# Performance work log

Hardware: AMD Instinct MI355X
Metric: run time of the kernel (lower is better)

## Reference

```python
import jax, jax.numpy as jnp
import numpy as np

N_GRAPHS = 512  # number of graphs in the batch
S2S_STEPS = 3   # Set2Set processing_steps


def segment_softmax(e, seg, num_seg):
    m = jax.ops.segment_max(e, seg, num_segments=num_seg)
    ex = jnp.exp(e - m[seg])
    s = jax.ops.segment_sum(ex, seg, num_segments=num_seg)
    return ex / s[seg]


def setup_inputs() -> dict:
    key = jax.random.key(0)
    ks = jax.random.split(key, 24)
    N, E, Fin, Fe, D = 30000, 480000, 25, 14, 256
    s = 0.05
    inp = {
        "x": jax.random.normal(ks[0], (N, Fin), jnp.float32),
        "edge_attr": jax.random.normal(ks[1], (E, Fe), jnp.float32),
        # lin0
        "W0": jax.random.normal(ks[2], (Fin, D), jnp.float32) * s,
        "b0": jnp.zeros((D,), jnp.float32),
        # DMPNN edge-message MLP: [x_src || e_attr] -> D -> D
        "Wm1": jax.random.normal(ks[3], (D + Fe, D), jnp.float32) * s,
        "bm1": jnp.zeros((D,), jnp.float32),
        "Wm2": jax.random.normal(ks[4], (D, D), jnp.float32) * s,
        "bm2": jnp.zeros((D,), jnp.float32),
        # node (root) update
        "Wr": jax.random.normal(ks[5], (D, D), jnp.float32) * s,
        "br": jnp.zeros((D,), jnp.float32),
        # Set2Set LSTM: input 2D -> hidden D
        "Wih": jax.random.normal(ks[6], (2 * D, 4 * D), jnp.float32) * s,
        "Whh": jax.random.normal(ks[7], (D, 4 * D), jnp.float32) * s,
        "bl": jnp.zeros((4 * D,), jnp.float32),
        # readout MLP
        "W1": jax.random.normal(ks[8], (2 * D, D), jnp.float32) * s,
        "b1": jnp.zeros((D,), jnp.float32),
        "W2": jax.random.normal(ks[9], (D, 1), jnp.float32) * s,
        "b2": jnp.zeros((1,), jnp.float32),
        "edge_index": jax.random.randint(ks[10], (2, E), 0, N, jnp.int32),
        "batch": jnp.sort(jax.random.randint(ks[11], (N,), 0, N_GRAPHS, jnp.int32)),
    }
    return inp


def reference(x, edge_attr, W0, b0, Wm1, bm1, Wm2, bm2, Wr, br,
              Wih, Whh, bl, W1, b1, W2, b2, edge_index, batch):
    N = x.shape[0]
    # lin0 + relu
    h0 = jax.nn.relu(x @ W0 + b0)  # [N, D]
    # DMPNNLayer2: edge-conditioned message, sum-aggregate, root update (eval: no dropout)
    src, dst = edge_index[0], edge_index[1]
    m = jax.nn.relu(jnp.concatenate([h0[src], edge_attr], axis=-1) @ Wm1 + bm1)  # [E, D]
    m = m @ Wm2 + bm2
    agg = jax.ops.segment_sum(m, dst, num_segments=N)  # [N, D]
    out = jax.nn.relu(h0 @ Wr + br + agg)  # relu in top-level forward, massage_depth=1
    # Set2Set pooling (processing_steps=3)
    D = out.shape[1]
    B = N_GRAPHS
    q_star = jnp.zeros((B, 2 * D), out.dtype)
    h = jnp.zeros((B, D), out.dtype)
    c = jnp.zeros((B, D), out.dtype)
    for _ in range(S2S_STEPS):
        gates = q_star @ Wih + h @ Whh + bl  # [B, 4D]
        i, f, g, o = jnp.split(gates, 4, axis=-1)
        c = jax.nn.sigmoid(f) * c + jax.nn.sigmoid(i) * jnp.tanh(g)
        h = jax.nn.sigmoid(o) * jnp.tanh(c)
        e = jnp.sum(out * h[batch], axis=-1)              # [N]
        a = segment_softmax(e, batch, B)                  # [N]
        r = jax.ops.segment_sum(a[:, None] * out, batch, num_segments=B)  # [B, D]
        q_star = jnp.concatenate([h, r], axis=-1)
    # readout (eval: dropout identity)
    y = jax.nn.relu(q_star @ W1 + b1)
    y = y @ W2 + b2
    return y.reshape(-1)
```

## Files before the change

### kernel.cpp

```cpp
#include <hip/hip_runtime.h>

typedef unsigned short u16;
typedef unsigned char u8;
typedef unsigned int u32;
using s16x8 = __attribute__((ext_vector_type(8))) short;
using f32x4 = __attribute__((ext_vector_type(4))) float;

#define DEV static __device__ __forceinline__

DEV float b2f(u16 u) { return __uint_as_float(((u32)u) << 16); }
DEV u16 f2bu(float f) {
    u32 u = __float_as_uint(f);
    u32 r = (u + 0x7FFFu + ((u >> 16) & 1u)) >> 16;
    return (u16)r;
}
DEV float sigm(float x) { return 1.0f / (1.0f + expf(-x)); }

DEV float ldv(const void* p, int i, int f32flag) {
    if (f32flag) return ((const float*)p)[i];
    return b2f(((const u16*)p)[i]);
}
DEV void stv(void* p, int i, float v, int f32flag) {
    if (f32flag) ((float*)p)[i] = v;
    else ((u16*)p)[i] = f2bu(v);
}

DEV int lower_bound(const int* b, int n, int v) {
    int lo = 0, hi = n;
    while (lo < hi) { int mid = (lo + hi) >> 1; if (b[mid] < v) lo = mid + 1; else hi = mid; }
    return lo;
}

__global__ void DMPNN_Change_678604832935_kernel(int* p) {
    if (p && threadIdx.x == 0 && blockIdx.x == 0) p[0] = 1;
}

__global__ void detect_kernel(const void* x, int* flag) {
    __shared__ int cnt[128];
    int tid = threadIdx.x;
    if (tid < 128) {
        u16 v = ((const u16*)x)[tid];
        int e = (v >> 7) & 0xFF;
        cnt[tid] = (e >= 100 && e <= 141) ? 1 : 0;
    }
    __syncthreads();
    if (tid == 0) {
        int s = 0;
        for (int i = 0; i < 128; ++i) s += cnt[i];
        flag[0] = (s < 110) ? 1 : 0;
    }
}

__global__ void fillv_kernel(void* out, const int* flag, float v) {
    int i = blockIdx.x * 256 + threadIdx.x;
    if (i < 512) stv(out, i, v, flag[0]);
}

__global__ void zero_kernel(float* p, int n) {
    int i = blockIdx.x * 256 + threadIdx.x;
    int stride = gridDim.x * 256;
    for (; i < n; i += stride) p[i] = 0.0f;
}

__global__ void hist_kernel(const int* __restrict__ eidx, u32* __restrict__ cnt) {
    int i = blockIdx.x * 256 + threadIdx.x;
    if (i < 480000) atomicAdd(&cnt[eidx[480000 + i]], 1u);
}

__global__ void scan1_kernel(const u32* __restrict__ cnt, u32* __restrict__ part) {
    __shared__ u32 s[256];
    int i = blockIdx.x * 256 + threadIdx.x;
    s[threadIdx.x] = (i < 30000) ? cnt[i] : 0u;
    __syncthreads();
    for (int st = 128; st > 0; st >>= 1) {
        if (threadIdx.x < st) s[threadIdx.x] += s[threadIdx.x + st];
        __syncthreads();
    }
    if (threadIdx.x == 0) part[blockIdx.x] = s[0];
}

__global__ void scan2_kernel(const u32* __restrict__ part, u32* __restrict__ pexcl, int nb) {
    if (threadIdx.x == 0 && blockIdx.x == 0) {
        u32 run = 0;
        for (int i = 0; i < nb; ++i) { pexcl[i] = run; run += part[i]; }
    }
}

__global__ void scan3_kernel(u32* __restrict__ cursor, const u32* __restrict__ pexcl) {
    __shared__ u32 s[256];
    int b = blockIdx.x, tid = threadIdx.x;
    int i = b * 256 + tid;
    u32 v = (i < 30000) ? cursor[i] : 0u;
    s[tid] = v;
    __syncthreads();
    for (int off = 1; off < 256; off <<= 1) {
        u32 t = (tid >= off) ? s[tid - off] : 0u;
        __syncthreads();
        s[tid] += t;
        __syncthreads();
    }
    u32 excl = s[tid] - v + pexcl[b];
    if (i < 30000) cursor[i] = excl;
}

__global__ void scatter_kernel(const int* __restrict__ eidx, u32* __restrict__ cursor,
                               u16* __restrict__ permLo, u8* __restrict__ permHi) {
    int i = blockIdx.x * 256 + threadIdx.x;
    if (i < 480000) {
        int d = eidx[480000 + i];
        u32 pos = atomicAdd(&cursor[d], 1u);
        permLo[pos] = (u16)(i & 0xFFFF);
        permHi[pos] = (u8)(i >> 16);
    }
}

__global__ void deg_kernel(const u32* __restrict__ cursor, float* __restrict__ degf) {
    int i = blockIdx.x * 256 + threadIdx.x;
    if (i < 30000) {
        u32 end = cursor[i];
        u32 beg = (i > 0) ? cursor[i - 1] : 0u;
        degf[i] = (float)(end - beg);
    }
}

__global__ void to_blocked(const void* src, int K, int ktiles, const int* flag,
                           u16* dst) {
    int idx = blockIdx.x * 256 + threadIdx.x;
    int total = ktiles * 4 * 256 * 8;
    if (idx >= total) return;
    int f32 = flag[0];
    int c = idx & 7;
    int n = (idx >> 3) & 255;
    int jk = idx >> 11;
    int j = jk & 3, kt = jk >> 2;
    int k = kt * 32 + j * 8 + c;
    u16 v = 0;
    if (k < K) v = f2bu(ldv(src, k * 256 + n, f32));
    dst[idx] = v;
}

__global__ void to_blocked2(const void* src1, int K1, const void* src2, int K2,
                            const int* flag, u16* dst) {
    int idx = blockIdx.x * 256 + threadIdx.x;
    int total = 24 * 4 * 1024 * 8;
    if (idx >= total) return;
    int f32 = flag[0];
    int c = idx & 7;
    int n = (idx >> 3) & 1023;
    int jk = idx >> 13;
    int j = jk & 3, kt = jk >> 2;
    int k = kt * 32 + j * 8 + c;
    u16 v = 0;
    if (k < K1) v = f2bu(ldv(src1, k * 1024 + n, f32));
    else if (k - K1 < K2) v = f2bu(ldv(src2, (k - K1) * 1024 + n, f32));
    dst[idx] = v;
}

__global__ __launch_bounds__(256) void lin0_kernel(const void* x, const void* W0,
                                                   const void* b0, const int* flag,
                                                   u16* h0b) {
    int f32 = flag[0];
    int n0 = blockIdx.x * 8, tid = threadIdx.x;
    __shared__ float xs[8][26];
    if (tid < 200) {
        int nn = tid / 25, k = tid % 25;
        xs[nn][k] = ldv(x, (n0 + nn) * 25 + k, f32);
    }
    __syncthreads();
    float wr[25];
    #pragma unroll
    for (int k = 0; k < 25; ++k) wr[k] = ldv(W0, k * 256 + tid, f32);
    float bias = ldv(b0, tid, f32);
    #pragma unroll
    for (int nn = 0; nn < 8; ++nn) {
        float a = bias;
        #pragma unroll
        for (int k = 0; k < 25; ++k) a += xs[nn][k] * wr[k];
        h0b[(n0 + nn) * 256 + tid] = f2bu(fmaxf(a, 0.0f));
    }
}

__global__ __launch_bounds__(256) void qgen_kernel(
    const u16* __restrict__ h0b, const u16* __restrict__ Wm1b,
    u16* __restrict__ Qb) {
    __shared__ __attribute__((aligned(16))) u16 As[64 * 264];
    const int tid = threadIdx.x;
    const int w = tid >> 6, lane = tid & 63, quad = lane >> 4, mrow = lane & 15;
    const int row0 = blockIdx.x * 64;
    const int colb = w * 64 + mrow;
    const int r = tid >> 2, sub = tid & 3;

    {
        int row = row0 + r;
        u16* arow = As + r * 264;
        #pragma unroll
        for (int j = 0; j < 8; ++j) {
            int c0 = sub * 64 + j * 8;
            s16x8 v = {0, 0, 0, 0, 0, 0, 0, 0};
            if (row < 30000) v = *(const s16x8*)(h0b + row * 256 + c0);
            *(s16x8*)(arow + c0) = v;
        }
    }
    __syncthreads();

    f32x4 acc[4][4];
    f32x4 fzero = {0.f, 0.f, 0.f, 0.f};
    #pragma unroll
    for (int mi = 0; mi < 4; ++mi)
        #pragma unroll
        for (int ni = 0; ni < 4; ++ni) acc[mi][ni] = fzero;

    for (int kt = 0; kt < 8; ++kt) {
        s16x8 af[4], bf[4];
        #pragma unroll
        for (int ni = 0; ni < 4; ++ni)
            bf[ni] = *(const s16x8*)(Wm1b + (((kt * 4 + quad) * 256) + colb + ni * 16) * 8);
        #pragma unroll
        for (int mi = 0; mi < 4; ++mi)
            af[mi] = *(const s16x8*)(As + (mi * 16 + mrow) * 264 + kt * 32 + quad * 8);
        #pragma unroll
        for (int mi = 0; mi < 4; ++mi)
            #pragma unroll
            for (int ni = 0; ni < 4; ++ni)
                acc[mi][ni] = __builtin_amdgcn_mfma_f32_16x16x32_bf16(af[mi], bf[ni], acc[mi][ni], 0, 0, 0);
    }

    #pragma unroll
    for (int mi = 0; mi < 4; ++mi)
        #pragma unroll
        for (int rg = 0; rg < 4; ++rg) {
            int row = row0 + mi * 16 + quad * 4 + rg;
            if (row >= 30000) continue;
            #pragma unroll
            for (int ni = 0; ni < 4; ++ni)
                Qb[row * 256 + colb + ni * 16] = f2bu(acc[mi][ni][rg]);
        }
}

#define MAXD 96
__global__ __launch_bounds__(256) void edge_mfma_node_kernel(
    const u16* __restrict__ Qb, const void* __restrict__ eattr,
    const int* __restrict__ eidx,
    const u16* __restrict__ permLo, const u8* __restrict__ permHi,
    const u32* __restrict__ cursor,
    const u16* __restrict__ Wm1b, const void* __restrict__ bm1,
    const int* __restrict__ flag, float* __restrict__ aggP) {
    const int f32 = flag[0];
    const int n = blockIdx.x, tid = threadIdx.x;
    const int w = tid >> 6, lane = tid & 63, quad = lane >> 4, mrow = lane & 15;
    const int beg = (n > 0) ? (int)cursor[n - 1] : 0;
    const int end = (int)cursor[n];
    __shared__ int eids[MAXD];
    __shared__ int sorted_s[MAXD];
    __shared__ int srcs16[16];
    __shared__ __attribute__((aligned(16))) u16 Ae[16 * 40];

    const int colb = w * 64 + mrow;
    s16x8 bf[4];
    float bm1c[4];
    #pragma unroll
    for (int ni = 0; ni < 4; ++ni) {
        bf[ni] = *(const s16x8*)(Wm1b + (((32 + quad) * 256) + colb + ni * 16) * 8);
        bm1c[ni] = ldv(bm1, colb + ni * 16, f32);
    }

    float psum[4] = {0.f, 0.f, 0.f, 0.f};
    const f32x4 fzero = {0.f, 0.f, 0.f, 0.f};

    for (int base = beg; base < end; base += MAXD) {
        int wcnt = end - base; if (wcnt > MAXD) wcnt = MAXD;
        if (tid < wcnt) {
            int si = base + tid;
            eids[tid] = (int)permLo[si] | ((int)permHi[si] << 16);
        }
        __syncthreads();
        if (tid < wcnt) {
            int key = eids[tid], r2 = 0;
            for (int j = 0; j < wcnt; ++j) r2 += (eids[j] < key);
            sorted_s[r2] = key;
        }
        __syncthreads();

        for (int cb = 0; cb < wcnt; cb += 16) {
            {
                int row = tid >> 4, c = tid & 15;
                int gi = cb + row;
                int e = (gi < wcnt) ? sorted_s[gi] : -1;
                u16 v = 0;
                if (e >= 0 && c < 14) v = f2bu(ldv(eattr, e * 14 + c, f32));
                Ae[row * 40 + c] = v;
                Ae[row * 40 + 16 + c] = 0;
                if (c == 0) srcs16[row] = (e >= 0) ? eidx[e] : 0;
            }
            __syncthreads();

            s16x8 af = *(const s16x8*)(Ae + mrow * 40 + quad * 8);
            f32x4 acc[4];
            #pragma unroll
            for (int ni = 0; ni < 4; ++ni)
                acc[ni] = __builtin_amdgcn_mfma_f32_16x16x32_bf16(af, bf[ni], fzero, 0, 0, 0);

            #pragma unroll
            for (int rg = 0; rg < 4; ++rg) {
                int row = quad * 4 + rg;
                if (cb + row < wcnt) {
                    const u16* qrow = Qb + srcs16[row] * 256;
                    #pragma unroll
                    for (int ni = 0; ni < 4; ++ni) {
                        float q = b2f(qrow[colb + ni * 16]);
                        psum[ni] += fmaxf(acc[ni][rg] + bm1c[ni] + q, 0.0f);
                    }
                }
            }
            __syncthreads();
        }
    }

    #pragma unroll
    for (int ni = 0; ni < 4; ++ni) {
        float v = psum[ni];
        v += __shfl_xor(v, 16, 64);
        v += __shfl_xor(v, 32, 64);
        psum[ni] = v;
    }
    if (quad == 0) {
        #pragma unroll
        for (int ni = 0; ni < 4; ++ni)
            aggP[n * 256 + colb + ni * 16] = psum[ni];
    }
}

__global__ __launch_bounds__(256) void edge_sorted_kernel(
    const u16* __restrict__ h0b, const void* __restrict__ eattr,
    const int* __restrict__ eidx,
    const u16* __restrict__ permLo, const u8* __restrict__ permHi,
    const u16* __restrict__ Wm1b,
    const void* __restrict__ bm1,
    const int* __restrict__ flag, float* __restrict__ aggP) {
    __shared__ __attribute__((aligned(16))) u16 As[64 * 296];
    __shared__ int dsh[64];
    const int f32 = flag[0];
    const int tid = threadIdx.x;
    const int w = tid >> 6, lane = tid & 63, quad = lane >> 4, mrow = lane & 15;
    const int eb0 = blockIdx.x * 64;
    const int colb = w * 64 + mrow;

    if (tid < 64) {
        int sj = eb0 + tid;
        int ee = (int)permLo[sj] | ((int)permHi[sj] << 16);
        dsh[tid] = eidx[480000 + ee];
    }
    {
        int r = tid >> 2, sub = tid & 3;
        int si = eb0 + r;
        int e = (int)permLo[si] | ((int)permHi[si] << 16);
        int src = eidx[e];
        const u16* hrow = h0b + src * 256;
        u16* arow = As + r * 296;
        #pragma unroll
        for (int j = 0; j < 8; ++j) {
            int c0 = sub * 64 + j * 8;
            *(s16x8*)(arow + c0) = *(const s16x8*)(hrow + c0);
        }
        if (sub == 0) {
            for (int c = 0; c < 14; ++c) arow[256 + c] = f2bu(ldv(eattr, e * 14 + c, f32));
            for (int c = 14; c < 40; ++c) arow[256 + c] = 0;
        }
    }
    __syncthreads();

    f32x4 acc[4][4];
    f32x4 fzero = {0.f, 0.f, 0.f, 0.f};
    #pragma unroll
    for (int mi = 0; mi < 4; ++mi)
        #pragma unroll
        for (int ni = 0; ni < 4; ++ni) acc[mi][ni] = fzero;

    for (int kt = 0; kt < 9; ++kt) {
        s16x8 af[4], bf[4];
        #pragma unroll
        for (int ni = 0; ni < 4; ++ni)
            bf[ni] = *(const s16x8*)(Wm1b + (((kt * 4 + quad) * 256) + colb + ni * 16) * 8);
        #pragma unroll
        for (int mi = 0; mi < 4; ++mi)
            af[mi] = *(const s16x8*)(As + (mi * 16 + mrow) * 296 + kt * 32 + quad * 8);
        #pragma unroll
        for (int mi = 0; mi < 4; ++mi)
            #pragma unroll
            for (int ni = 0; ni < 4; ++ni)
                acc[mi][ni] = __builtin_amdgcn_mfma_f32_16x16x32_bf16(af[mi], bf[ni], acc[mi][ni], 0, 0, 0);
    }

    float bm1c[4];
    #pragma unroll
    for (int ni = 0; ni < 4; ++ni) bm1c[ni] = ldv(bm1, colb + ni * 16, f32);
    __syncthreads();
    #pragma unroll
    for (int mi = 0; mi < 4; ++mi)
        #pragma unroll
        for (int ni = 0; ni < 4; ++ni)
            #pragma unroll
            for (int rg = 0; rg < 4; ++rg) {
                int row = mi * 16 + quad * 4 + rg;
                As[row * 296 + colb + ni * 16] = f2bu(fmaxf(acc[mi][ni][rg] + bm1c[ni], 0.0f));
            }
    __syncthreads();

    {
        int c = tid;
        float s = 0.0f;
        int cur = dsh[0];
        #pragma unroll 8
        for (int rr = 0; rr < 64; ++rr) {
            int d = dsh[rr];
            if (d != cur) { atomicAdd(&aggP[cur * 256 + c], s); s = 0.0f; cur = d; }
            s += b2f(As[rr * 296 + c]);
        }
        atomicAdd(&aggP[cur * 256 + c], s);
    }
}

__global__ __launch_bounds__(256) void node_dual_kernel(
    u16* __restrict__ h0b, const u16* __restrict__ Wrb, const u16* __restrict__ Wm2b,
    const void* __restrict__ br, const void* __restrict__ bm2,
    const float* __restrict__ aggP, const float* __restrict__ degf,
    const int* __restrict__ flag) {
    __shared__ __attribute__((aligned(16))) u16 As[64 * 264];
    const int f32 = flag[0];
    const int tid = threadIdx.x;
    const int w = tid >> 6, lane = tid & 63, quad = lane >> 4, mrow = lane & 15;
    const int row0 = blockIdx.x * 64;
    const int colb = w * 64 + mrow;
    const int r = tid >> 2, sub = tid & 3;

    {
        int row = row0 + r;
        u16* arow = As + r * 264;
        #pragma unroll
        for (int j = 0; j < 8; ++j) {
            int c0 = sub * 64 + j * 8;
            s16x8 v = {0, 0, 0, 0, 0, 0, 0, 0};
            if (row < 30000) v = *(const s16x8*)(h0b + row * 256 + c0);
            *(s16x8*)(arow + c0) = v;
        }
    }
    __syncthreads();

    f32x4 acc[4][4];
    f32x4 fzero = {0.f, 0.f, 0.f, 0.f};
    #pragma unroll
    for (int mi = 0; mi < 4; ++mi)
        #pragma unroll
        for (int ni = 0; ni < 4; ++ni) acc[mi][ni] = fzero;

    for (int kt = 0; kt < 8; ++kt) {
        s16x8 af[4], bf[4];
        #pragma unroll
        for (int ni = 0; ni < 4; ++ni)
            bf[ni] = *(const s16x8*)(Wrb + (((kt * 4 + quad) * 256) + colb + ni * 16) * 8);
        #pragma unroll
        for (int mi = 0; mi < 4; ++mi)
            af[mi] = *(const s16x8*)(As + (mi * 16 + mrow) * 264 + kt * 32 + quad * 8);
        #pragma unroll
        for (int mi = 0; mi < 4; ++mi)
            #pragma unroll
            for (int ni = 0; ni < 4; ++ni)
                acc[mi][ni] = __builtin_amdgcn_mfma_f32_16x16x32_bf16(af[mi], bf[ni], acc[mi][ni], 0, 0, 0);
    }
    __syncthreads();

    {
        int row = row0 + r;
        u16* arow = As + r * 264;
        #pragma unroll
        for (int j = 0; j < 8; ++j) {
            int c0 = sub * 64 + j * 8;
            s16x8 pk = {0, 0, 0, 0, 0, 0, 0, 0};
            if (row < 30000) {
                f32x4 a = *(const f32x4*)(aggP + row * 256 + c0);
                f32x4 b = *(const f32x4*)(aggP + row * 256 + c0 + 4);
                pk[0] = (short)f2bu(a[0]); pk[1] = (short)f2bu(a[1]);
                pk[2] = (short)f2bu(a[2]); pk[3] = (short)f2bu(a[3]);
                pk[4] = (short)f2bu(b[0]); pk[5] = (short)f2bu(b[1]);
                pk[6] = (short)f2bu(b[2]); pk[7] = (short)f2bu(b[3]);
            }
            *(s16x8*)(arow + c0) = pk;
        }
    }
    __syncthreads();

    for (int kt = 0; kt < 8; ++kt) {
        s16x8 af[4], bf[4];
        #pragma unroll
        for (int ni = 0; ni < 4; ++ni)
            bf[ni] = *(const s16x8*)(Wm2b + (((kt * 4 + quad) * 256) + colb + ni * 16) * 8);
        #pragma unroll
        for (int mi = 0; mi < 4; ++mi)
            af[mi] = *(const s16x8*)(As + (mi * 16 + mrow) * 264 + kt * 32 + quad * 8);
        #pragma unroll
        for (int mi = 0; mi < 4; ++mi)
            #pragma unroll
            for (int ni = 0; ni < 4; ++ni)
                acc[mi][ni] = __builtin_amdgcn_mfma_f32_16x16x32_bf16(af[mi], bf[ni], acc[mi][ni], 0, 0, 0);
    }

    #pragma unroll
    for (int mi = 0; mi < 4; ++mi)
        #pragma unroll
        for (int rg = 0; rg < 4; ++rg) {
            int row = row0 + mi * 16 + quad * 4 + rg;
            if (row >= 30000) continue;
            float dg = degf[row];
            #pragma unroll
            for (int ni = 0; ni < 4; ++ni) {
                int col = colb + ni * 16;
                float v = acc[mi][ni][rg] + ldv(br, col, f32) + dg * ldv(bm2, col, f32);
                h0b[row * 256 + col] = f2bu(fmaxf(v, 0.0f));
            }
        }
}

__global__ __launch_bounds__(256) void gates_mfma_kernel(
    const u16* __restrict__ Abuf, const u16* __restrict__ Wcatb,
    float* __restrict__ G) {
    const int tid = threadIdx.x;
    const int w = tid >> 6, lane = tid & 63, quad = lane >> 4, mrow = lane & 15;
    const int row0 = blockIdx.x * 64;
    const int col = blockIdx.y * 64 + w * 16 + mrow;

    f32x4 acc[4];
    f32x4 fzero = {0.f, 0.f, 0.f, 0.f};
    #pragma unroll
    for (int mi = 0; mi < 4; ++mi) acc[mi] = fzero;

    for (int kt = 0; kt < 24; ++kt) {
        s16x8 bfv = *(const s16x8*)(Wcatb + (((kt * 4 + quad) * 1024) + col) * 8);
        s16x8 af[4];
        #pragma unroll
        for (int mi = 0; mi < 4; ++mi)
            af[mi] = *(const s16x8*)(Abuf + (row0 + mi * 16 + mrow) * 768 + kt * 32 + quad * 8);
        #pragma unroll
        for (int mi = 0; mi < 4; ++mi)
            acc[mi] = __builtin_amdgcn_mfma_f32_16x16x32_bf16(af[mi], bfv, acc[mi], 0, 0, 0);
    }

    #pragma unroll
    for (int mi = 0; mi < 4; ++mi)
        #pragma unroll
        for (int rg = 0; rg < 4; ++rg)
            G[(row0 + mi * 16 + quad * 4 + rg) * 1024 + col] = acc[mi][rg];
}

__global__ __launch_bounds__(256) void lstm_kernel(const float* G, const void* bl,
                                                   const int* flag,
                                                   float* Cst, float* Hst,
                                                   u16* Abuf) {
    int f32 = flag[0];
    int b = blockIdx.x, d = threadIdx.x;
    float gi = G[b * 1024 + d]       + ldv(bl, d, f32);
    float gf = G[b * 1024 + 256 + d] + ldv(bl, 256 + d, f32);
    float gg = G[b * 1024 + 512 + d] + ldv(bl, 512 + d, f32);
    float go = G[b * 1024 + 768 + d] + ldv(bl, 768 + d, f32);
    float c = Cst[b * 256 + d];
    c = sigm(gf) * c + sigm(gi) * tanhf(gg);
    Cst[b * 256 + d] = c;
    float h = sigm(go) * tanhf(c);
    Hst[b * 256 + d] = h;
    u16 hb = f2bu(h);
    Abuf[b * 768 + d] = hb;
    Abuf[b * 768 + 512 + d] = hb;
}

__global__ __launch_bounds__(256) void e_kernel(const u16* outb, const float* Hst,
                                                const int* batch, float* ebuf) {
    __shared__ float part[8][33];
    int tid = threadIdx.x;
    int g8 = tid >> 5, l = tid & 31;
    for (int n0 = blockIdx.x * 8; n0 < 30000; n0 += gridDim.x * 8) {
        int n = n0 + g8;
        float p = 0.0f;
        if (n < 30000) {
            int g = batch[n];
            const u16* orow = outb + n * 256 + l * 8;
            const float* hrow = Hst + g * 256 + l * 8;
            #pragma unroll
            for (int c = 0; c < 8; ++c) p += b2f(orow[c]) * hrow[c];
        }
        part[g8][l] = p;
        __syncthreads();
        if (tid < 8) {
            int n2 = n0 + tid;
            if (n2 < 30000) {
                float s = 0.0f;
                #pragma unroll
                for (int i = 0; i < 32; ++i) s += part[tid][i];
                ebuf[n2] = s;
            }
        }
        __syncthreads();
    }
}

__global__ __launch_bounds__(256) void graph_kernel(const float* ebuf, const u16* outb,
                                                    const int* batch, float* Rst,
                                                    u16* Abuf) {
    int b = blockIdx.x, tid = threadIdx.x;
    int n0 = lower_bound(batch, 30000, b);
    int n1 = lower_bound(batch, 30000, b + 1);
    __shared__ float red[256];
    __shared__ float pb[256];
    float r_out = 0.0f;
    if (n1 > n0) {
        float m = -1e30f;
        for (int n = n0 + tid; n < n1; n += 256) m = fmaxf(m, ebuf[n]);
        red[tid] = m; __syncthreads();
        for (int s = 128; s > 0; s >>= 1) { if (tid < s) red[tid] = fmaxf(red[tid], red[tid + s]); __syncthreads(); }
        m = red[0]; __syncthreads();
        float sl = 0.0f;
        for (int n = n0 + tid; n < n1; n += 256) sl += expf(ebuf[n] - m);
        red[tid] = sl; __syncthreads();
        for (int s = 128; s > 0; s >>= 1) { if (tid < s) red[tid] += red[tid + s]; __syncthreads(); }
        float ssum = red[0]; __syncthreads();
        float acc = 0.0f;
        for (int c0 = n0; c0 < n1; c0 += 256) {
            int nn = n1 - c0; if (nn > 256) nn = 256;
            __syncthreads();
            if (tid < nn) pb[tid] = expf(ebuf[c0 + tid] - m);
            __syncthreads();
            for (int i = 0; i < nn; ++i) acc += pb[i] * b2f(outb[(c0 + i) * 256 + tid]);
        }
        r_out = acc / ssum;
    }
    Rst[b * 256 + tid] = r_out;
    Abuf[b * 768 + 256 + tid] = f2bu(r_out);
}

__global__ __launch_bounds__(256) void readout_kernel(const float* Hst, const float* Rst,
                                                      const void* W1, const void* b1,
                                                      const void* W2, const void* b2,
                                                      const u16* nodeout, const float* aggP,
                                                      const int* flag, void* out) {
    int f32 = flag[0];
    int b = blockIdx.x, tid = threadIdx.x;
    __shared__ float qs[512];
    __shared__ float red[256];
    qs[tid] = Hst[b * 256 + tid];
    qs[256 + tid] = Rst[b * 256 + tid];
    __syncthreads();
    float a = ldv(b1, tid, f32);
    for (int k = 0; k < 512; ++k) a += qs[k] * ldv(W1, k * 256 + tid, f32);
    a = fmaxf(a, 0.0f) * ldv(W2, tid, f32);
    red[tid] = a; __syncthreads();
    for (int s = 128; s > 0; s >>= 1) { if (tid < s) red[tid] += red[tid + s]; __syncthreads(); }
    if (tid == 0) {
        float D = 0.0f;
        if (b == 0) {
            float s1 = 0.0f, s2 = 0.0f, s3 = 0.0f;
            for (int i = 0; i < 256; ++i) {
                s1 += fabsf(b2f(nodeout[i]));
                s2 += fabsf(aggP[i]);
                s3 += fabsf(Rst[i]);
            }
            if (s1 < 1e-3f) D += 100.0f;
            if (s2 < 1e-3f) D += 200.0f;
            if (s3 < 1e-6f) D += 400.0f;
        }
        stv(out, b, red[0] + ldv(b2, 0, f32) + D, f32);
    }
}

#define OFF_FLAG 0
#define OFF_HST  64
#define OFF_RST  524352
#define OFF_CST  1048640
#define OFF_PLO  64
#define OFF_PHI  960064
#define OFF_CUR  1440064
#define OFF_WREG 1572928
#define OFF_WM1B (OFF_WREG)
#define OFF_WM2B (OFF_WREG + 147456)
#define OFF_WRB  (OFF_WREG + 278528)
#define OFF_WCAT (OFF_WREG + 409600)
#define OFF_E    3670080
#define OFF_AGG  3790144
#define OFF_ABUF (OFF_AGG + 1048576)
#define OFF_G    (OFF_AGG + 4194304)
#define OFF_H0B  34510144
#define WS_NEEDED 49870144
#define OFF_Q    49870144
#define WS_FAST  (49870144 + 15360000)

extern "C" __attribute__((visibility("default")))
void kernel_launch(void* const* d_in, const int* in_sizes, int n_in,
                   void* d_out, int out_size, void* d_ws, size_t ws_size,
                   hipStream_t stream) {
    char* ws = (char*)d_ws;
    int*   flag   = (int*)(ws + OFF_FLAG);
    float* Hst    = (float*)(ws + OFF_HST);
    float* Rst    = (float*)(ws + OFF_RST);
    float* Cst    = (float*)(ws + OFF_CST);
    u16*   permLo = (u16*)(ws + OFF_PLO);
    u8*    permHi = (u8*)(ws + OFF_PHI);
    u32*   cursor = (u32*)(ws + OFF_CUR);
    u16*   Wm1b   = (u16*)(ws + OFF_WM1B);
    u16*   Wm2b   = (u16*)(ws + OFF_WM2B);
    u16*   Wrb    = (u16*)(ws + OFF_WRB);
    u16*   Wcatb  = (u16*)(ws + OFF_WCAT);
    float* ebuf   = (float*)(ws + OFF_E);
    u32*   part   = (u32*)(ws + OFF_E);
    u32*   pexcl  = (u32*)(ws + OFF_E + 512);
    float* degf   = (float*)(ws + OFF_E);
    float* aggP   = (float*)(ws + OFF_AGG);
    u16*   Abuf   = (u16*)(ws + OFF_ABUF);
    float* G      = (float*)(ws + OFF_G);
    u16*   h0b    = (u16*)(ws + OFF_H0B);
    u16*   Qb     = (u16*)(ws + OFF_Q);

    detect_kernel<<<1, 256, 0, stream>>>(d_in[0], flag);

    bool sizes_ok = (n_in == 19)
        && in_sizes[0] == 30000 * 25
        && in_sizes[1] == 480000 * 14
        && in_sizes[4] == 270 * 256
        && in_sizes[10] == 512 * 1024
        && in_sizes[17] == 2 * 480000
        && in_sizes[18] == 30000;
    if (!sizes_ok) { fillv_kernel<<<2, 256, 0, stream>>>(d_out, flag, 1600.0f); return; }
    if (ws_size < (size_t)WS_NEEDED) { fillv_kernel<<<2, 256, 0, stream>>>(d_out, flag, 800.0f); return; }
    const bool fast = (ws_size >= (size_t)WS_FAST);

    fillv_kernel<<<2, 256, 0, stream>>>(d_out, flag, 3.0f);
    DMPNN_Change_678604832935_kernel<<<1, 64, 0, stream>>>((int*)(ws + OFF_G));

    const void* x     = d_in[0];
    const void* eattr = d_in[1];
    const void* W0    = d_in[2];
    const void* b0    = d_in[3];
    const void* Wm1   = d_in[4];
    const void* bm1   = d_in[5];
    const void* Wm2   = d_in[6];
    const void* bm2   = d_in[7];
    const void* Wr    = d_in[8];
    const void* br    = d_in[9];
    const void* Wih   = d_in[10];
    const void* Whh   = d_in[11];
    const void* bl    = d_in[12];
    const void* W1    = d_in[13];
    const void* b1    = d_in[14];
    const void* W2    = d_in[15];
    const void* b2    = d_in[16];
    const int* eidx   = (const int*)d_in[17];
    const int* batch  = (const int*)d_in[18];

    to_blocked<<<288, 256, 0, stream>>>(Wm1, 270, 9, flag, Wm1b);
    to_blocked<<<256, 256, 0, stream>>>(Wm2, 256, 8, flag, Wm2b);
    to_blocked<<<256, 256, 0, stream>>>(Wr, 256, 8, flag, Wrb);
    to_blocked2<<<3072, 256, 0, stream>>>(Wih, 512, Whh, 256, flag, Wcatb);

    lin0_kernel<<<3750, 256, 0, stream>>>(x, W0, b0, flag, h0b);

    zero_kernel<<<30, 256, 0, stream>>>((float*)cursor, 30000);
    hist_kernel<<<1875, 256, 0, stream>>>(eidx, cursor);
    scan1_kernel<<<118, 256, 0, stream>>>(cursor, part);
    scan2_kernel<<<1, 64, 0, stream>>>(part, pexcl, 118);
    scan3_kernel<<<118, 256, 0, stream>>>(cursor, pexcl);
    scatter_kernel<<<1875, 256, 0, stream>>>(eidx, cursor, permLo, permHi);
    deg_kernel<<<118, 256, 0, stream>>>(cursor, degf);

    if (fast) {
        qgen_kernel<<<469, 256, 0, stream>>>(h0b, Wm1b, Qb);
        edge_mfma_node_kernel<<<30000, 256, 0, stream>>>(Qb, eattr, eidx, permLo, permHi,
                                                         cursor, Wm1b, bm1, flag, aggP);
    } else {
        zero_kernel<<<1024, 256, 0, stream>>>(aggP, 7680000);
        edge_sorted_kernel<<<7500, 256, 0, stream>>>(h0b, eattr, eidx, permLo, permHi,
                                                     Wm1b, bm1, flag, aggP);
    }
    node_dual_kernel<<<469, 256, 0, stream>>>(h0b, Wrb, Wm2b, br, bm2, aggP, degf, flag);

    zero_kernel<<<64, 256, 0, stream>>>(Cst, 131072);
    zero_kernel<<<64, 256, 0, stream>>>((float*)Abuf, 196608);

    for (int s = 0; s < 3; ++s) {
        gates_mfma_kernel<<<dim3(8, 16), 256, 0, stream>>>(Abuf, Wcatb, G);
        lstm_kernel<<<512, 256, 0, stream>>>(G, bl, flag, Cst, Hst, Abuf);
        e_kernel<<<512, 256, 0, stream>>>(h0b, Hst, batch, ebuf);
        graph_kernel<<<512, 256, 0, stream>>>(ebuf, h0b, batch, Rst, Abuf);
    }
    readout_kernel<<<512, 256, 0, stream>>>(Hst, Rst, W1, b1, W2, b2, h0b, aggP, flag, d_out);
}
```

Baseline: 509.1 us.

## Fuse Set2Set attention score and softmax-pooling kernels with LDS-staged node rows

```diff
diff --git a/kernel.cpp b/kernel.cpp
--- a/kernel.cpp
+++ b/kernel.cpp
@@ -4,6 +4,7 @@
 typedef unsigned char u8;
 typedef unsigned int u32;
 using s16x8 = __attribute__((ext_vector_type(8))) short;
+using s16x4 = __attribute__((ext_vector_type(4))) short;
 using f32x4 = __attribute__((ext_vector_type(4))) float;
 
 #define DEV static __device__ __forceinline__
@@ -571,46 +572,63 @@
     Abuf[b * 768 + 512 + d] = hb;
 }
 
-__global__ __launch_bounds__(256) void e_kernel(const u16* outb, const float* Hst,
-                                                const int* batch, float* ebuf) {
-    __shared__ float part[8][33];
-    int tid = threadIdx.x;
-    int g8 = tid >> 5, l = tid & 31;
-    for (int n0 = blockIdx.x * 8; n0 < 30000; n0 += gridDim.x * 8) {
-        int n = n0 + g8;
-        float p = 0.0f;
-        if (n < 30000) {
-            int g = batch[n];
-            const u16* orow = outb + n * 256 + l * 8;
-            const float* hrow = Hst + g * 256 + l * 8;
-            #pragma unroll
-            for (int c = 0; c < 8; ++c) p += b2f(orow[c]) * hrow[c];
-        }
-        part[g8][l] = p;
+#define GROWS 112
+__global__ __launch_bounds__(256) void s2s_fused_kernel(
+    const u16* __restrict__ outb, const float* __restrict__ Hst,
+    const int* __restrict__ batch, float* __restrict__ Rst,
+    u16* __restrict__ Abuf, float* __restrict__ ebuf) {
+    __shared__ __attribute__((aligned(16))) u16 Ls[GROWS * 256];
+    __shared__ __attribute__((aligned(16))) float hsh[256];
+    __shared__ float esh[GROWS];
+    __shared__ float red[256];
+    const int b = blockIdx.x, tid = threadIdx.x;
+    const int w = tid >> 6, lane = tid & 63;
+    const int n0 = lower_bound(batch, 30000, b);
+    const int n1 = lower_bound(batch, 30000, b + 1);
+    const int cnt = n1 - n0;
+    hsh[tid] = Hst[b * 256 + tid];
+    __syncthreads();
+    float r_out = 0.0f;
+    if (cnt > 0 && cnt <= GROWS) {
+        for (int idx = tid; idx < cnt * 32; idx += 256) {
+            int i = idx >> 5, c8 = idx & 31;
+            *(s16x8*)(Ls + i * 256 + c8 * 8) = *(const s16x8*)(outb + (n0 + i) * 256 + c8 * 8);
+        }
         __syncthreads();
-        if (tid < 8) {
-            int n2 = n0 + tid;
-            if (n2 < 30000) {
-                float s = 0.0f;
-                #pragma unroll
-                for (int i = 0; i < 32; ++i) s += part[tid][i];
-                ebuf[n2] = s;
-            }
+        for (int i = w; i < cnt; i += 4) {
+            s16x4 ov = *(const s16x4*)(Ls + i * 256 + lane * 4);
+            f32x4 hv = *(const f32x4*)(hsh + lane * 4);
+            float p = b2f((u16)ov[0]) * hv[0] + b2f((u16)ov[1]) * hv[1]
+                    + b2f((u16)ov[2]) * hv[2] + b2f((u16)ov[3]) * hv[3];
+            #pragma unroll
+            for (int off = 1; off < 64; off <<= 1) p += __shfl_xor(p, off, 64);
+            if (lane == 0) esh[i] = p;
         }
         __syncthreads();
-    }
-}
-
-__global__ __launch_bounds__(256) void graph_kernel(const float* ebuf, const u16* outb,
-                                                    const int* batch, float* Rst,
-                                                    u16* Abuf) {
-    int b = blockIdx.x, tid = threadIdx.x;
-    int n0 = lower_bound(batch, 30000, b);
-    int n1 = lower_bound(batch, 30000, b + 1);
-    __shared__ float red[256];
-    __shared__ float pb[256];
-    float r_out = 0.0f;
-    if (n1 > n0) {
+        float m = -1e30f;
+        for (int i = tid; i < cnt; i += 256) m = fmaxf(m, esh[i]);
+        red[tid] = m; __syncthreads();
+        for (int s = 128; s > 0; s >>= 1) { if (tid < s) red[tid] = fmaxf(red[tid], red[tid + s]); __syncthreads(); }
+        m = red[0]; __syncthreads();
+        float sl = 0.0f;
+        for (int i = tid; i < cnt; i += 256) { float pe = expf(esh[i] - m); esh[i] = pe; sl += pe; }
+        red[tid] = sl; __syncthreads();
+        for (int s = 128; s > 0; s >>= 1) { if (tid < s) red[tid] += red[tid + s]; __syncthreads(); }
+        float ssum = red[0]; __syncthreads();
+        float acc = 0.0f;
+        for (int i = 0; i < cnt; ++i) acc += esh[i] * b2f(Ls[i * 256 + tid]);
+        r_out = acc / ssum;
+    } else if (cnt > GROWS) {
+        for (int i = w; i < cnt; i += 4) {
+            const u16* orow = outb + (n0 + i) * 256 + lane * 4;
+            f32x4 hv = *(const f32x4*)(hsh + lane * 4);
+            float p = b2f(orow[0]) * hv[0] + b2f(orow[1]) * hv[1]
+                    + b2f(orow[2]) * hv[2] + b2f(orow[3]) * hv[3];
+            #pragma unroll
+            for (int off = 1; off < 64; off <<= 1) p += __shfl_xor(p, off, 64);
+            if (lane == 0) ebuf[n0 + i] = p;
+        }
+        __syncthreads();
         float m = -1e30f;
         for (int n = n0 + tid; n < n1; n += 256) m = fmaxf(m, ebuf[n]);
         red[tid] = m; __syncthreads();
@@ -625,9 +643,9 @@
         for (int c0 = n0; c0 < n1; c0 += 256) {
             int nn = n1 - c0; if (nn > 256) nn = 256;
             __syncthreads();
-            if (tid < nn) pb[tid] = expf(ebuf[c0 + tid] - m);
+            if (tid < nn) red[tid] = expf(ebuf[c0 + tid] - m);
             __syncthreads();
-            for (int i = 0; i < nn; ++i) acc += pb[i] * b2f(outb[(c0 + i) * 256 + tid]);
+            for (int i = 0; i < nn; ++i) acc += red[i] * b2f(outb[(c0 + i) * 256 + tid]);
         }
         r_out = acc / ssum;
     }
@@ -784,8 +802,7 @@
     for (int s = 0; s < 3; ++s) {
         gates_mfma_kernel<<<dim3(8, 16), 256, 0, stream>>>(Abuf, Wcatb, G);
         lstm_kernel<<<512, 256, 0, stream>>>(G, bl, flag, Cst, Hst, Abuf);
-        e_kernel<<<512, 256, 0, stream>>>(h0b, Hst, batch, ebuf);
-        graph_kernel<<<512, 256, 0, stream>>>(ebuf, h0b, batch, Rst, Abuf);
+        s2s_fused_kernel<<<512, 256, 0, stream>>>(h0b, Hst, batch, Rst, Abuf, ebuf);
     }
     readout_kernel<<<512, 256, 0, stream>>>(Hst, Rst, W1, b1, W2, b2, h0b, aggP, flag, d_out);
 }
```

Result: no change. 506.3 us (-0.5%).
